# Kernel optimization log

Hardware: AMD Instinct MI355X
Metric: run time of the kernel (lower is better)

Reference implementation:

```python
import jax, jax.numpy as jnp
import numpy as np

def mexican_hat(z):
    z2 = z * z
    return (1.0 - z2) * jnp.exp(-0.5 * z2)

def setup_inputs() -> dict:
    key = jax.random.key(0)
    k1, k2 = jax.random.split(key)
    B, N, D = 8192, 512, 64
    x = jax.random.normal(k1, (B, D), dtype=jnp.float32)
    centers = jax.random.normal(k2, (N, D), dtype=jnp.float32)
    scales = jnp.ones((N, D), dtype=jnp.float32)
    return {"x": x, "centers": centers, "scales": scales}

def reference(x, centers, scales):
    # x: (B, D); centers/scales: (N, D)
    z = (x[:, None, :] - centers[None, :, :]) / scales[None, :, :]  # (B, N, D)
    psi = mexican_hat(z)
    h = jnp.prod(psi, axis=2)  # (B, N)
    return h
```

## Files before the change

kernel.cpp:

```cpp
#include <hip/hip_runtime.h>


#define DD 64

typedef float v4f __attribute__((ext_vector_type(4)));

__global__ __launch_bounds__(256)
void prep(const float* __restrict__ c, const float* __restrict__ s,
          float2* __restrict__ pq, int total) {
    int i = blockIdx.x * 256 + threadIdx.x;
    if (i < total) {
        float r = 1.0f / s[i];
        pq[i] = make_float2(c[i] * r, r);
    }
}

__global__ __launch_bounds__(256, 2)
void wavelet_kernel(const float* __restrict__ x,
                    const float2* __restrict__ pq,
                    float* __restrict__ out, int B, int N) {
    __shared__ __align__(16) char pool[32 * 1024 + 4 * 64 * 17 * 4];
    float* xs = (float*)pool;
    v4f*   par = (v4f*)pool;
    float* ol = (float*)(pool + 32 * 1024);

    int t = threadIdx.x;
    int lane = t & 63;
    int wv = __builtin_amdgcn_readfirstlane(t >> 6);
    int bblk = blockIdx.x * 64;
    int nblk = blockIdx.y * 64;

    {
        const float4* xg = (const float4*)(x + (size_t)bblk * DD);
#pragma unroll
        for (int j = 0; j < 4; ++j) {
            int idx = j * 256 + t;
            int row = idx >> 4, c4 = idx & 15;
            float4 v = xg[idx];
            float* p = &xs[row * 65 + c4 * 4];
            p[0] = v.x; p[1] = v.y; p[2] = v.z; p[3] = v.w;
        }
    }
    __syncthreads();

    float xr[DD];
#pragma unroll
    for (int d = 0; d < DD; ++d) xr[d] = xs[lane * 65 + d];
    __syncthreads();

    {
        const v4f* pg = (const v4f*)(pq + (size_t)nblk * DD);
#pragma unroll
        for (int j = 0; j < 8; ++j) par[j * 256 + t] = pg[j * 256 + t];
    }
    __syncthreads();

    const v4f* Pw = par + (size_t)(wv * 16) * 32;
#pragma unroll 1
    for (int ni = 0; ni < 16; ++ni) {
        const v4f* Pn = Pw + ni * 32;
        float acc = 1.0f;
#pragma unroll
        for (int k = 0; k < 4; ++k) {
            float p = 1.0f, s2 = 0.0f;
#pragma unroll
            for (int i = 0; i < 8; ++i) {
                v4f q = Pn[k * 8 + i];
                float z0 = __builtin_fmaf(xr[k * 16 + 2 * i], q.y, -q.x);
                float z1 = __builtin_fmaf(xr[k * 16 + 2 * i + 1], q.w, -q.z);
                float w0 = z0 * z0;
                float w1 = z1 * z1;
                p = __builtin_fmaf(-w0, p, p);
                p = __builtin_fmaf(-w1, p, p);
                s2 += w0;
                s2 += w1;
            }
            acc *= p * __builtin_exp2f(-0.72134752f * s2);
        }
        ol[(wv * 64 + lane) * 17 + ni] = acc;
    }

#pragma unroll
    for (int g = 0; g < 4; ++g) {
        int row = (lane >> 2) + 16 * g;
        int col = (lane & 3) * 4;
        const float* l = &ol[(wv * 64 + row) * 17 + col];
        float4 v = make_float4(l[0], l[1], l[2], l[3]);
        float* orow = out + (size_t)(bblk + row) * N + nblk + wv * 16 + col;
        *(float4*)orow = v;
    }
}

extern "C" void kernel_launch(void* const* d_in, const int* in_sizes, int n_in,
                              void* d_out, int out_size, void* d_ws, size_t ws_size,
                              hipStream_t stream) {
    const float* x = (const float*)d_in[0];
    const float* c = (const float*)d_in[1];
    const float* s = (const float*)d_in[2];
    float* out = (float*)d_out;

    int B = in_sizes[0] / DD;
    int N = in_sizes[1] / DD;

    float2* pq = (float2*)d_ws;

    int total = N * DD;
    prep<<<(total + 255) / 256, 256, 0, stream>>>(c, s, pq, total);

    dim3 grid(B / 64, N / 64);
    wavelet_kernel<<<grid, 256, 0, stream>>>(x, pq, out, B, N);
}
```

Baseline: 98.31 us.

## Fuse center/scale prep into main kernel and write outputs directly

Removes the separate prep kernel and computes c/s and 1/s inside each block while staging parameters into shared memory, which saves a launch and a global round trip. It also drops the LDS output transpose: each lane now writes its 16 results straight to global memory with strided scalar stores. The k loop is no longer unrolled, which cuts code size and register pressure but adds loop overhead. The scalar stores are less coalesced than the old float4 writes, and every block now redoes the reciprocal work.

```diff
diff --git a/kernel.cpp b/kernel.cpp
--- a/kernel.cpp
+++ b/kernel.cpp
@@ -5,24 +5,14 @@
 
 typedef float v4f __attribute__((ext_vector_type(4)));
 
-__global__ __launch_bounds__(256)
-void prep(const float* __restrict__ c, const float* __restrict__ s,
-          float2* __restrict__ pq, int total) {
-    int i = blockIdx.x * 256 + threadIdx.x;
-    if (i < total) {
-        float r = 1.0f / s[i];
-        pq[i] = make_float2(c[i] * r, r);
-    }
-}
-
 __global__ __launch_bounds__(256, 2)
-void wavelet_kernel(const float* __restrict__ x,
-                    const float2* __restrict__ pq,
-                    float* __restrict__ out, int B, int N) {
-    __shared__ __align__(16) char pool[32 * 1024 + 4 * 64 * 17 * 4];
+void wavelet_fused(const float* __restrict__ x,
+                   const float* __restrict__ c,
+                   const float* __restrict__ s,
+                   float* __restrict__ out, int B, int N) {
+    __shared__ __align__(16) char pool[32 * 1024];
     float* xs = (float*)pool;
-    v4f*   par = (v4f*)pool;
-    float* ol = (float*)(pool + 32 * 1024);
+    v4f* par = (v4f*)pool;
 
     int t = threadIdx.x;
     int lane = t & 63;
@@ -49,18 +39,26 @@
     __syncthreads();
 
     {
-        const v4f* pg = (const v4f*)(pq + (size_t)nblk * DD);
+        const float2* cg = (const float2*)(c + (size_t)nblk * DD);
+        const float2* sg = (const float2*)(s + (size_t)nblk * DD);
 #pragma unroll
-        for (int j = 0; j < 8; ++j) par[j * 256 + t] = pg[j * 256 + t];
+        for (int j = 0; j < 8; ++j) {
+            int i = j * 256 + t;
+            float2 cc = cg[i];
+            float2 ss = sg[i];
+            float r0 = 1.0f / ss.x;
+            float r1 = 1.0f / ss.y;
+            par[i] = (v4f){cc.x * r0, r0, cc.y * r1, r1};
+        }
     }
     __syncthreads();
 
-    const v4f* Pw = par + (size_t)(wv * 16) * 32;
+    float* orow = out + (size_t)(bblk + lane) * N + nblk + wv * 16;
 #pragma unroll 1
     for (int ni = 0; ni < 16; ++ni) {
-        const v4f* Pn = Pw + ni * 32;
+        const v4f* Pn = par + (wv * 16 + ni) * 32;
         float acc = 1.0f;
-#pragma unroll
+#pragma unroll 1
         for (int k = 0; k < 4; ++k) {
             float p = 1.0f, s2 = 0.0f;
 #pragma unroll
@@ -77,17 +75,7 @@
             }
             acc *= p * __builtin_exp2f(-0.72134752f * s2);
         }
-        ol[(wv * 64 + lane) * 17 + ni] = acc;
-    }
-
-#pragma unroll
-    for (int g = 0; g < 4; ++g) {
-        int row = (lane >> 2) + 16 * g;
-        int col = (lane & 3) * 4;
-        const float* l = &ol[(wv * 64 + row) * 17 + col];
-        float4 v = make_float4(l[0], l[1], l[2], l[3]);
-        float* orow = out + (size_t)(bblk + row) * N + nblk + wv * 16 + col;
-        *(float4*)orow = v;
+        orow[ni] = acc;
     }
 }
 
@@ -102,11 +90,8 @@
     int B = in_sizes[0] / DD;
     int N = in_sizes[1] / DD;
 
-    float2* pq = (float2*)d_ws;
-
-    int total = N * DD;
-    prep<<<(total + 255) / 256, 256, 0, stream>>>(c, s, pq, total);
+    (void)d_ws; (void)ws_size;
 
     dim3 grid(B / 64, N / 64);
-    wavelet_kernel<<<grid, 256, 0, stream>>>(x, pq, out, B, N);
+    wavelet_fused<<<grid, 256, 0, stream>>>(x, c, s, out, B, N);
 }
```

Result: slower. 246.0 us (+150.2%).
